# Kernel optimization log

Measured on AMD Instinct MI355X. Metric: run time of the kernel, lower is better.

Reference implementation:

```python
import jax, jax.numpy as jnp
from jax import lax
import numpy as np

BINS = 256

def setup_inputs() -> dict:
    key = jax.random.key(0)
    k1, k2 = jax.random.split(key)
    B, C, H, W = 8, 3, 1024, 1024
    dst = jax.random.uniform(k1, (B, C, H, W), dtype=jnp.float32)
    ref = jax.random.uniform(k2, (B, C, H, W), dtype=jnp.float32)
    return {"dst": dst, "ref": ref}


def _cal_hist(img):
    # img: [B,C,H,W] in [0,1]. torch.histc(img*255, bins=256, min=0, max=255):
    # bin width = 255/256, so bin = floor(img*255 / (255/256)) = floor(img*256).
    # Inputs are in [0,1) so nothing is out of histc's range (clip is a no-op safeguard).
    B, C, H, W = img.shape
    bc = B * C
    x = img.reshape(bc, H * W)
    idx = jnp.clip(jnp.floor(x * float(BINS)).astype(jnp.int32), 0, BINS - 1)
    rows = jnp.arange(bc, dtype=jnp.int32)[:, None]
    counts = jnp.zeros((bc, BINS), jnp.float32).at[rows, idx].add(1.0)
    # F.normalize(p=1, dim=1) with eps=1e-12
    counts = counts / jnp.maximum(jnp.sum(counts, axis=1, keepdims=True), 1e-12)
    # triu-bmm == cumulative sum -> per-channel CDF
    return jnp.cumsum(counts, axis=1)


def _trans_row(cdf_dst, cdf_ref):
    # Faithful vectorization of the sequential two-pointer loop in cal_trans.
    # For each i (pointer j only ever advances): match at the smallest
    # j' >= j with cdf_ref[j'-1] <= d <= cdf_ref[j']; if impossible, j runs
    # off to 256 and this and all later entries become 255.
    def step(j, d):
        s = jnp.searchsorted(cdf_ref, d)            # smallest s with cdf_ref[s] >= d, in [0,256]
        cand = jnp.maximum(j, s)                    # pointer never moves backwards; cand in [1,256]
        ok = (j < BINS) & (cand <= BINS - 1) & (d >= cdf_ref[cand - 1])
        out = jnp.where(ok, cand, BINS - 1)
        j_next = jnp.where(ok, cand, jnp.int32(BINS))
        return j_next, out.astype(jnp.int32)
    _, tail = lax.scan(step, jnp.int32(1), cdf_dst[1:])  # i = 1..255
    table = jnp.concatenate([jnp.zeros(1, jnp.int32), tail])  # table[0] = arange init = 0
    return table.at[BINS - 1].set(BINS - 1)                   # table[:,255] = 255


def reference(dst, ref):
    B, C, H, W = dst.shape
    bc = B * C
    hist_dst = _cal_hist(dst)   # [BC,256] CDFs
    hist_ref = _cal_hist(ref)
    tables = jax.vmap(_trans_row)(hist_dst, hist_ref)  # [BC,256] int32
    # NOTE: original code indexes tables[b*c] (not b*C+c) -- bug preserved faithfully.
    b_idx = jnp.arange(B, dtype=jnp.int32)[:, None]
    c_idx = jnp.arange(C, dtype=jnp.int32)[None, :]
    row_sel = (b_idx * c_idx).reshape(-1)               # [BC]
    luts = tables[row_sel]                              # [BC,256]
    pix = jnp.clip((dst * 255.0).astype(jnp.int32), 0, BINS - 1).reshape(bc, H * W)
    rst = jnp.take_along_axis(luts, pix, axis=1).reshape(B, C, H, W)
    return rst.astype(dst.dtype) / 255.0
```

## Files before the change

kernel.cpp:

```cpp
#include <hip/hip_runtime.h>

#define BINS 256
#define BC_N 24
#define C_N  3
#define NROWS 12
#define CH   64
#define WAVES 4

__global__ __launch_bounds__(256) void hm_hist(const float* __restrict__ dst,
                                               const float* __restrict__ refp,
                                               unsigned int* __restrict__ hist,
                                               int n4_per_row) {
    __shared__ unsigned int shist[BINS];
    __shared__ unsigned int wsum[WAVES][BINS];

    const int t = threadIdx.x;
    const int l = t & 63;
    const int w = t >> 6;

    shist[t] = 0u;
    __syncthreads();

    const int y = blockIdx.y;
    const int row = (y < 9) ? y : 2 * y - 8;
    const float* img = blockIdx.z ? refp : dst;
    const float4* p = reinterpret_cast<const float4*>(img) + (size_t)row * n4_per_row;

    const unsigned long long t0 = (l & 1)  ? 0ull : ~0ull;
    const unsigned long long t1 = (l & 2)  ? 0ull : ~0ull;
    const unsigned long long t2 = (l & 4)  ? 0ull : ~0ull;
    const unsigned long long t3 = (l & 8)  ? 0ull : ~0ull;
    const unsigned long long t4 = (l & 16) ? 0ull : ~0ull;
    const unsigned long long t5 = (l & 32) ? 0ull : ~0ull;
    unsigned int c0 = 0, c1 = 0, c2 = 0, c3 = 0;

    auto grp = [&](float x) {
        int bin = min((int)(x * 256.0f), BINS - 1);
        unsigned long long B0 = __ballot(bin & 1);
        unsigned long long B1 = __ballot(bin & 2);
        unsigned long long B2 = __ballot(bin & 4);
        unsigned long long B3 = __ballot(bin & 8);
        unsigned long long B4 = __ballot(bin & 16);
        unsigned long long B5 = __ballot(bin & 32);
        unsigned long long B6 = __ballot(bin & 64);
        unsigned long long B7 = __ballot(bin & 128);
        unsigned long long m = (B0 ^ t0) & (B1 ^ t1) & (B2 ^ t2)
                             & (B3 ^ t3) & (B4 ^ t4) & (B5 ^ t5);
        unsigned long long a = m & ~B7, b = m & B7;
        c0 += (unsigned)__popcll(a & ~B6);
        c1 += (unsigned)__popcll(a &  B6);
        c2 += (unsigned)__popcll(b & ~B6);
        c3 += (unsigned)__popcll(b &  B6);
    };
    auto atom = [&](float x) {
        atomicAdd(&shist[min((int)(x * 256.0f), BINS - 1)], 1u);
    };

    const int stride = CH * 256;
    const int nfull = n4_per_row / (8 * stride);
    int i = blockIdx.x * 256 + t;

    for (int it = 0; it < nfull; ++it, i += 8 * stride) {
        float4 v[8];
        #pragma unroll
        for (int k = 0; k < 8; ++k) v[k] = p[i + k * stride];
        __builtin_amdgcn_sched_barrier(0);
        #pragma unroll
        for (int k = 0; k < 4; ++k) {
            atom(v[k].x); atom(v[k].y); atom(v[k].z); atom(v[k].w);
        }
        #pragma unroll
        for (int k = 4; k < 8; ++k) {
            grp(v[k].x); grp(v[k].y); grp(v[k].z); grp(v[k].w);
        }
    }
    for (int j = nfull * 8 * stride + blockIdx.x * 256 + t; j < n4_per_row; j += stride) {
        float4 v = p[j];
        atom(v.x); atom(v.y); atom(v.z); atom(v.w);
    }
    __syncthreads();

    wsum[w][l]       = c0;
    wsum[w][l + 64]  = c1;
    wsum[w][l + 128] = c2;
    wsum[w][l + 192] = c3;
    __syncthreads();

    unsigned int s = shist[t] + wsum[0][t] + wsum[1][t] + wsum[2][t] + wsum[3][t];
    unsigned int* g = hist + ((size_t)blockIdx.z * NROWS + y) * BINS;
    atomicAdd(&g[t], s);
}

__global__ __launch_bounds__(256) void hm_table(const unsigned int* __restrict__ hist,
                                                float* __restrict__ lut) {
    __shared__ unsigned int sd[BINS], sr[BINS];
    __shared__ float cdf_d[BINS], cdf_r[BINS];
    __shared__ int firstFail;

    const int r = blockIdx.x;
    const int t = threadIdx.x;

    unsigned int xd = hist[(size_t)r * BINS + t];
    unsigned int xr = hist[(size_t)(NROWS + r) * BINS + t];
    if (t == 0) firstFail = BINS;
    sd[t] = xd; sr[t] = xr;
    __syncthreads();

    #pragma unroll
    for (int off = 1; off < BINS; off <<= 1) {
        unsigned int yd = (t >= off) ? sd[t - off] : 0u;
        unsigned int yr = (t >= off) ? sr[t - off] : 0u;
        __syncthreads();
        xd += yd; xr += yr;
        sd[t] = xd; sr[t] = xr;
        __syncthreads();
    }
    float totd = fmaxf((float)sd[BINS - 1], 1e-12f);
    float totr = fmaxf((float)sr[BINS - 1], 1e-12f);
    cdf_d[t] = (float)xd / totd;
    cdf_r[t] = (float)xr / totr;
    __syncthreads();

    int out;
    if (t == 0) {
        out = 0;
    } else {
        float d = cdf_d[t];
        int lo = 0, hi = BINS;
        while (lo < hi) {
            int m = (lo + hi) >> 1;
            if (cdf_r[m] < d) lo = m + 1; else hi = m;
        }
        int cand = lo > 1 ? lo : 1;
        bool ok = (cand <= BINS - 1) && (d >= cdf_r[cand - 1]);
        if (!ok) atomicMin(&firstFail, t);
        out = cand;
    }
    __syncthreads();

    if (t >= firstFail) out = BINS - 1;
    if (t == BINS - 1) out = BINS - 1;
    lut[(size_t)r * BINS + t] = (float)out / 255.0f;
}

__global__ __launch_bounds__(256) void hm_apply(const float* __restrict__ dst,
                                                const float* __restrict__ lut,
                                                float* __restrict__ out,
                                                int n4_per_row) {
    __shared__ float slut[BINS];
    const int bc = blockIdx.y;
    const int b = bc / C_N;
    const int c = bc - b * C_N;
    const int r = b * c;
    const int cr = (r <= 8) ? r : 8 + ((r - 8) >> 1);
    const int t = threadIdx.x;

    slut[t] = lut[(size_t)cr * BINS + t];
    __syncthreads();

    const float4* in4 = reinterpret_cast<const float4*>(dst) + (size_t)bc * n4_per_row;
    float4* out4 = reinterpret_cast<float4*>(out) + (size_t)bc * n4_per_row;
    const int gsz = gridDim.x * blockDim.x;

    #pragma unroll 4
    for (int i = blockIdx.x * blockDim.x + t; i < n4_per_row; i += gsz) {
        float4 v = in4[i];
        float4 o;
        o.x = slut[min(max((int)(v.x * 255.0f), 0), BINS - 1)];
        o.y = slut[min(max((int)(v.y * 255.0f), 0), BINS - 1)];
        o.z = slut[min(max((int)(v.z * 255.0f), 0), BINS - 1)];
        o.w = slut[min(max((int)(v.w * 255.0f), 0), BINS - 1)];
        out4[i] = o;
    }
}

extern "C" void kernel_launch(void* const* d_in, const int* in_sizes, int n_in,
                              void* d_out, int out_size, void* d_ws, size_t ws_size,
                              hipStream_t stream) {
    const float* dst  = (const float*)d_in[0];
    const float* refp = (const float*)d_in[1];
    float* out = (float*)d_out;

    const int total = in_sizes[0];
    const int hw = total / BC_N;
    const int n4 = hw >> 2;

    unsigned int* hist = (unsigned int*)d_ws;
    float* lut = (float*)((char*)d_ws + (size_t)2 * NROWS * BINS * sizeof(unsigned int));

    hipMemsetAsync(d_ws, 0, (size_t)2 * NROWS * BINS * sizeof(unsigned int), stream);

    dim3 hg(CH, NROWS, 2);
    hm_hist<<<hg, dim3(256), 0, stream>>>(dst, refp, hist, n4);

    hm_table<<<dim3(NROWS), dim3(256), 0, stream>>>(hist, lut);

    dim3 ag(64, BC_N);
    hm_apply<<<ag, dim3(256), 0, stream>>>(dst, lut, out, n4);
}
```

Before: 73.10 us.

## Split histogram waves by role and write per-block partials instead of atomics

The histogram kernel now gives each block a contiguous span. Two waves handle roughly 9/16 of the 64-wide slices with shared-memory atomics, and the other two waves use ballot-based counting with a one-ahead prefetch. Each block writes its partial histogram to its own workspace slot, so the global atomics and the memset launch go away. The table kernel then sums the 64 partials per row. The cost is a larger workspace and extra reads in the table kernel, and the fixed atomic/ballot split may leave the waves unevenly loaded.

Measured after the change: 71.89 us. Within noise of the previous version (-1.7%).

```diff
diff --git a/kernel.cpp b/kernel.cpp
--- a/kernel.cpp
+++ b/kernel.cpp
@@ -5,93 +5,111 @@
 #define C_N  3
 #define NROWS 12
 #define CH   64
-#define WAVES 4
 
 __global__ __launch_bounds__(256) void hm_hist(const float* __restrict__ dst,
                                                const float* __restrict__ refp,
-                                               unsigned int* __restrict__ hist,
+                                               unsigned int* __restrict__ part,
                                                int n4_per_row) {
     __shared__ unsigned int shist[BINS];
-    __shared__ unsigned int wsum[WAVES][BINS];
+    __shared__ unsigned int wsum[2][BINS];
 
     const int t = threadIdx.x;
     const int l = t & 63;
     const int w = t >> 6;
 
     shist[t] = 0u;
+    wsum[0][t] = 0u; wsum[1][t] = 0u;
     __syncthreads();
 
     const int y = blockIdx.y;
     const int row = (y < 9) ? y : 2 * y - 8;
     const float* img = blockIdx.z ? refp : dst;
-    const float4* p = reinterpret_cast<const float4*>(img) + (size_t)row * n4_per_row;
-
-    const unsigned long long t0 = (l & 1)  ? 0ull : ~0ull;
-    const unsigned long long t1 = (l & 2)  ? 0ull : ~0ull;
-    const unsigned long long t2 = (l & 4)  ? 0ull : ~0ull;
-    const unsigned long long t3 = (l & 8)  ? 0ull : ~0ull;
-    const unsigned long long t4 = (l & 16) ? 0ull : ~0ull;
-    const unsigned long long t5 = (l & 32) ? 0ull : ~0ull;
-    unsigned int c0 = 0, c1 = 0, c2 = 0, c3 = 0;
-
-    auto grp = [&](float x) {
-        int bin = min((int)(x * 256.0f), BINS - 1);
-        unsigned long long B0 = __ballot(bin & 1);
-        unsigned long long B1 = __ballot(bin & 2);
-        unsigned long long B2 = __ballot(bin & 4);
-        unsigned long long B3 = __ballot(bin & 8);
-        unsigned long long B4 = __ballot(bin & 16);
-        unsigned long long B5 = __ballot(bin & 32);
-        unsigned long long B6 = __ballot(bin & 64);
-        unsigned long long B7 = __ballot(bin & 128);
-        unsigned long long m = (B0 ^ t0) & (B1 ^ t1) & (B2 ^ t2)
-                             & (B3 ^ t3) & (B4 ^ t4) & (B5 ^ t5);
-        unsigned long long a = m & ~B7, b = m & B7;
-        c0 += (unsigned)__popcll(a & ~B6);
-        c1 += (unsigned)__popcll(a &  B6);
-        c2 += (unsigned)__popcll(b & ~B6);
-        c3 += (unsigned)__popcll(b &  B6);
-    };
-    auto atom = [&](float x) {
-        atomicAdd(&shist[min((int)(x * 256.0f), BINS - 1)], 1u);
-    };
-
-    const int stride = CH * 256;
-    const int nfull = n4_per_row / (8 * stride);
-    int i = blockIdx.x * 256 + t;
-
-    for (int it = 0; it < nfull; ++it, i += 8 * stride) {
-        float4 v[8];
-        #pragma unroll
-        for (int k = 0; k < 8; ++k) v[k] = p[i + k * stride];
-        __builtin_amdgcn_sched_barrier(0);
-        #pragma unroll
-        for (int k = 0; k < 4; ++k) {
-            atom(v[k].x); atom(v[k].y); atom(v[k].z); atom(v[k].w);
-        }
-        #pragma unroll
-        for (int k = 4; k < 8; ++k) {
-            grp(v[k].x); grp(v[k].y); grp(v[k].z); grp(v[k].w);
-        }
-    }
-    for (int j = nfull * 8 * stride + blockIdx.x * 256 + t; j < n4_per_row; j += stride) {
-        float4 v = p[j];
-        atom(v.x); atom(v.y); atom(v.z); atom(v.w);
-    }
-    __syncthreads();
-
-    wsum[w][l]       = c0;
-    wsum[w][l + 64]  = c1;
-    wsum[w][l + 128] = c2;
-    wsum[w][l + 192] = c3;
-    __syncthreads();
-
-    unsigned int s = shist[t] + wsum[0][t] + wsum[1][t] + wsum[2][t] + wsum[3][t];
-    unsigned int* g = hist + ((size_t)blockIdx.z * NROWS + y) * BINS;
-    atomicAdd(&g[t], s);
-}
-
-__global__ __launch_bounds__(256) void hm_table(const unsigned int* __restrict__ hist,
+    const int span = n4_per_row / CH;
+    const float4* p = reinterpret_cast<const float4*>(img)
+                    + (size_t)row * n4_per_row + (size_t)blockIdx.x * span;
+
+    const int nsl = span >> 6;
+    const int NA  = (nsl * 9) >> 4;
+
+    if (w < 2) {
+        for (int s = w; s < NA; s += 2) {
+            float4 v = p[(s << 6) + l];
+            atomicAdd(&shist[min((int)(v.x * 256.0f), BINS - 1)], 1u);
+            atomicAdd(&shist[min((int)(v.y * 256.0f), BINS - 1)], 1u);
+            atomicAdd(&shist[min((int)(v.z * 256.0f), BINS - 1)], 1u);
+            atomicAdd(&shist[min((int)(v.w * 256.0f), BINS - 1)], 1u);
+        }
+        if (w == 0) {
+            for (int j = (nsl << 6) + l; j < span; j += 64) {
+                float4 v = p[j];
+                atomicAdd(&shist[min((int)(v.x * 256.0f), BINS - 1)], 1u);
+                atomicAdd(&shist[min((int)(v.y * 256.0f), BINS - 1)], 1u);
+                atomicAdd(&shist[min((int)(v.z * 256.0f), BINS - 1)], 1u);
+                atomicAdd(&shist[min((int)(v.w * 256.0f), BINS - 1)], 1u);
+            }
+            if (blockIdx.x == CH - 1) {
+                for (int j = CH * span + l; j < n4_per_row; j += 64) {
+                    const float4* pr = reinterpret_cast<const float4*>(img)
+                                     + (size_t)row * n4_per_row;
+                    float4 v = pr[j];
+                    atomicAdd(&shist[min((int)(v.x * 256.0f), BINS - 1)], 1u);
+                    atomicAdd(&shist[min((int)(v.y * 256.0f), BINS - 1)], 1u);
+                    atomicAdd(&shist[min((int)(v.z * 256.0f), BINS - 1)], 1u);
+                    atomicAdd(&shist[min((int)(v.w * 256.0f), BINS - 1)], 1u);
+                }
+            }
+        }
+    } else {
+        const unsigned long long t0 = (l & 1)  ? 0ull : ~0ull;
+        const unsigned long long t1 = (l & 2)  ? 0ull : ~0ull;
+        const unsigned long long t2 = (l & 4)  ? 0ull : ~0ull;
+        const unsigned long long t3 = (l & 8)  ? 0ull : ~0ull;
+        const unsigned long long t4 = (l & 16) ? 0ull : ~0ull;
+        const unsigned long long t5 = (l & 32) ? 0ull : ~0ull;
+        unsigned int c0 = 0, c1 = 0, c2 = 0, c3 = 0;
+
+        auto grp = [&](float x) {
+            int bin = min((int)(x * 256.0f), BINS - 1);
+            unsigned long long B0 = __ballot(bin & 1);
+            unsigned long long B1 = __ballot(bin & 2);
+            unsigned long long B2 = __ballot(bin & 4);
+            unsigned long long B3 = __ballot(bin & 8);
+            unsigned long long B4 = __ballot(bin & 16);
+            unsigned long long B5 = __ballot(bin & 32);
+            unsigned long long B6 = __ballot(bin & 64);
+            unsigned long long B7 = __ballot(bin & 128);
+            unsigned long long m = (B0 ^ t0) & (B1 ^ t1) & (B2 ^ t2)
+                                 & (B3 ^ t3) & (B4 ^ t4) & (B5 ^ t5);
+            unsigned long long a = m & ~B7, b = m & B7;
+            c0 += (unsigned)__popcll(a & ~B6);
+            c1 += (unsigned)__popcll(a &  B6);
+            c2 += (unsigned)__popcll(b & ~B6);
+            c3 += (unsigned)__popcll(b &  B6);
+        };
+
+        int s = NA + (w - 2);
+        if (s < nsl) {
+            float4 v = p[(s << 6) + l];
+            for (; s + 2 < nsl; s += 2) {
+                float4 nv = p[((s + 2) << 6) + l];
+                __builtin_amdgcn_sched_barrier(0);
+                grp(v.x); grp(v.y); grp(v.z); grp(v.w);
+                v = nv;
+            }
+            grp(v.x); grp(v.y); grp(v.z); grp(v.w);
+        }
+        wsum[w - 2][l]       = c0;
+        wsum[w - 2][l + 64]  = c1;
+        wsum[w - 2][l + 128] = c2;
+        wsum[w - 2][l + 192] = c3;
+    }
+    __syncthreads();
+
+    unsigned int sv = shist[t] + wsum[0][t] + wsum[1][t];
+    part[(((size_t)blockIdx.z * NROWS + y) * CH + blockIdx.x) * BINS + t] = sv;
+}
+
+__global__ __launch_bounds__(256) void hm_table(const unsigned int* __restrict__ part,
                                                 float* __restrict__ lut) {
     __shared__ unsigned int sd[BINS], sr[BINS];
     __shared__ float cdf_d[BINS], cdf_r[BINS];
@@ -100,8 +118,14 @@
     const int r = blockIdx.x;
     const int t = threadIdx.x;
 
-    unsigned int xd = hist[(size_t)r * BINS + t];
-    unsigned int xr = hist[(size_t)(NROWS + r) * BINS + t];
+    const unsigned int* pd = part + ((size_t)0 * NROWS + r) * CH * BINS;
+    const unsigned int* pr = part + ((size_t)1 * NROWS + r) * CH * BINS;
+    unsigned int xd = 0, xr = 0;
+    #pragma unroll 8
+    for (int k = 0; k < CH; ++k) {
+        xd += pd[k * BINS + t];
+        xr += pr[k * BINS + t];
+    }
     if (t == 0) firstFail = BINS;
     sd[t] = xd; sr[t] = xr;
     __syncthreads();
@@ -185,15 +209,13 @@
     const int hw = total / BC_N;
     const int n4 = hw >> 2;
 
-    unsigned int* hist = (unsigned int*)d_ws;
-    float* lut = (float*)((char*)d_ws + (size_t)2 * NROWS * BINS * sizeof(unsigned int));
-
-    hipMemsetAsync(d_ws, 0, (size_t)2 * NROWS * BINS * sizeof(unsigned int), stream);
+    unsigned int* part = (unsigned int*)d_ws;
+    float* lut = (float*)((char*)d_ws + (size_t)2 * NROWS * CH * BINS * sizeof(unsigned int));
 
     dim3 hg(CH, NROWS, 2);
-    hm_hist<<<hg, dim3(256), 0, stream>>>(dst, refp, hist, n4);
-
-    hm_table<<<dim3(NROWS), dim3(256), 0, stream>>>(hist, lut);
+    hm_hist<<<hg, dim3(256), 0, stream>>>(dst, refp, part, n4);
+
+    hm_table<<<dim3(NROWS), dim3(256), 0, stream>>>(part, lut);
 
     dim3 ag(64, BC_N);
     hm_apply<<<ag, dim3(256), 0, stream>>>(dst, lut, out, n4);
```
